# Performance work log

Measured on AMD Instinct MI355X. Metric: run time of the kernel, lower is better.

Reference implementation:

```python
import jax, jax.numpy as jnp
import numpy as np

HIDDEN = 1024
HEADS = 16
HEAD_DIM = HIDDEN // HEADS


def setup_inputs() -> dict:
    key = jax.random.key(0)
    ks = jax.random.split(key, 9)
    s = 1.0 / np.sqrt(HIDDEN)
    x = jax.random.normal(ks[0], (2, 2048, HIDDEN), dtype=jnp.float32)
    Wq = jax.random.uniform(ks[1], (HIDDEN, HIDDEN), jnp.float32, -s, s)
    bq = jax.random.uniform(ks[2], (HIDDEN,), jnp.float32, -s, s)
    Wk = jax.random.uniform(ks[3], (HIDDEN, HIDDEN), jnp.float32, -s, s)
    bk = jax.random.uniform(ks[4], (HIDDEN,), jnp.float32, -s, s)
    Wv = jax.random.uniform(ks[5], (HIDDEN, HIDDEN), jnp.float32, -s, s)
    bv = jax.random.uniform(ks[6], (HIDDEN,), jnp.float32, -s, s)
    Wo = jax.random.uniform(ks[7], (HIDDEN, HIDDEN), jnp.float32, -s, s)
    bo = jax.random.uniform(ks[8], (HIDDEN,), jnp.float32, -s, s)
    return {"x": x, "Wq": Wq, "bq": bq, "Wk": Wk, "bk": bk,
            "Wv": Wv, "bv": bv, "Wo": Wo, "bo": bo}


def reference(x, Wq, bq, Wk, bk, Wv, bv, Wo, bo):
    bs, seq_len, _ = x.shape
    # projections; weights stored as (in, out) so y = x @ W + b
    def proj(W, b):
        y = x @ W + b  # [bs, seq, hidden]
        return y.reshape(bs, seq_len, HEADS, HEAD_DIM).transpose(0, 2, 1, 3)  # [bs, h, seq, hd]
    q = proj(Wq, bq)
    k = proj(Wk, bk)
    v = proj(Wv, bv)
    scale = 1.0 / jnp.sqrt(jnp.float32(HEAD_DIM))
    scores = jnp.einsum('bhqd,bhkd->bhqk', q, k) * scale  # [bs, h, seq, seq]
    attn = jax.nn.softmax(scores, axis=-1)
    ctx = jnp.einsum('bhqk,bhkd->bhqd', attn, v)
    ctx = ctx.transpose(0, 2, 1, 3).reshape(bs, seq_len, HIDDEN)
    return ctx @ Wo + bo
```

## Files before the change

### kernel.cpp

```cpp
#include <hip/hip_runtime.h>
#include <hip/hip_bf16.h>

#define HDN 1024
#define NH  16
#define DH  64
#define NB  2
#define SQL 2048
#define MT  (NB*SQL)

using bf16 = __hip_bfloat16;
typedef __attribute__((ext_vector_type(8))) short s16x8;
typedef __attribute__((ext_vector_type(4))) float f32x4;
typedef __attribute__((ext_vector_type(16))) float f32x16;
typedef unsigned int u32;

__device__ __forceinline__ void gload_lds16(const void* g, void* l) {
  __builtin_amdgcn_global_load_lds((const __attribute__((address_space(1))) void*)g,
                                   (__attribute__((address_space(3))) void*)l, 16, 0, 0);
}

__device__ __forceinline__ unsigned short bfb(float f) {
  union { __hip_bfloat16 h; unsigned short u; } c;
  c.h = __float2bfloat16(f);
  return c.u;
}

__device__ __forceinline__ u32 cvtpk(float lo, float hi) {
  u32 r;
  asm("v_cvt_pk_bf16_f32 %0, %1, %2" : "=v"(r) : "v"(lo), "v"(hi));
  return r;
}

__global__ __launch_bounds__(256) void k_cvt_x(const float* __restrict__ x, bf16* __restrict__ xb) {
  int i = (blockIdx.x * 256 + threadIdx.x) * 8;
  float4 a = *(const float4*)(x + i);
  float4 b = *(const float4*)(x + i + 4);
  union { unsigned short u[8]; uint4 v; } o;
  o.u[0]=bfb(a.x); o.u[1]=bfb(a.y); o.u[2]=bfb(a.z); o.u[3]=bfb(a.w);
  o.u[4]=bfb(b.x); o.u[5]=bfb(b.y); o.u[6]=bfb(b.z); o.u[7]=bfb(b.w);
  *(uint4*)((unsigned short*)xb + i) = o.v;
}

__global__ __launch_bounds__(256) void k_trw(const float* __restrict__ Wq, const float* __restrict__ Wk,
                                             const float* __restrict__ Wv, const float* __restrict__ Wo,
                                             bf16* __restrict__ WqkvT, bf16* __restrict__ WoT) {
  __shared__ float tile[64][65];
  int z = blockIdx.z;
  const float* W = (z==0)?Wq:(z==1)?Wk:(z==2)?Wv:Wo;
  bf16* Wt = (z<3) ? (WqkvT + (size_t)z*HDN*HDN) : WoT;
  int r0 = blockIdx.y*64, c0 = blockIdx.x*64;
  int t = threadIdx.x, tr = t>>4, tc = (t&15)*4;
  #pragma unroll
  for (int p=0;p<4;p++){
    int r = p*16+tr;
    float4 v = *(const float4*)(W + (size_t)(r0+r)*HDN + c0 + tc);
    tile[r][tc]=v.x; tile[r][tc+1]=v.y; tile[r][tc+2]=v.z; tile[r][tc+3]=v.w;
  }
  __syncthreads();
  #pragma unroll
  for (int p=0;p<4;p++){
    int o = p*16+tr;
    union { unsigned short u[4]; ushort4 v; } pk;
    #pragma unroll
    for (int j=0;j<4;j++) pk.u[j] = bfb(tile[tc+j][o]);
    *(ushort4*)((unsigned short*)Wt + (size_t)(c0+o)*HDN + r0 + tc) = pk.v;
  }
}

template<int MODE>
__global__ __launch_bounds__(256,2) void k_gemm(
    const bf16* __restrict__ A, const bf16* __restrict__ B,
    const float* __restrict__ b0, const float* __restrict__ b1, const float* __restrict__ b2,
    bf16* __restrict__ oq, bf16* __restrict__ ok, bf16* __restrict__ ovt, float* __restrict__ oo) {
  constexpr int KD = 1024;
  __shared__ __align__(16) bf16 As[128*64];
  __shared__ __align__(16) bf16 Bs[128*64];
  int tid = threadIdx.x, lane = tid&63, wave = tid>>6;
  int g = lane>>4, lr = lane&15;
  int m0 = blockIdx.y*128, n0 = blockIdx.x*128;
  int wm = (wave>>1)*64, wn = (wave&1)*64;
  f32x4 acc[4][4] = {};
  for (int k0=0; k0<KD; k0+=64) {
    #pragma unroll
    for (int i=0;i<4;i++){
      int seg = wave*4+i;
      int flat = seg*64 + lane;
      int row = flat>>3, ch = flat&7;
      gload_lds16(A + (size_t)(m0+row)*KD + k0 + ch*8, (char*)As + seg*1024);
      gload_lds16(B + (size_t)(n0+row)*KD + k0 + ch*8, (char*)Bs + seg*1024);
    }
    __syncthreads();
    #pragma unroll
    for (int kk=0;kk<2;kk++){
      s16x8 af[4], bfg[4];
      #pragma unroll
      for (int mi=0;mi<4;mi++)
        af[mi] = *(const s16x8*)((const char*)As + (wm+mi*16+lr)*128 + kk*64 + g*16);
      #pragma unroll
      for (int ni=0;ni<4;ni++)
        bfg[ni] = *(const s16x8*)((const char*)Bs + (wn+ni*16+lr)*128 + kk*64 + g*16);
      #pragma unroll
      for (int mi=0;mi<4;mi++)
        #pragma unroll
        for (int ni=0;ni<4;ni++)
          acc[mi][ni] = __builtin_amdgcn_mfma_f32_16x16x32_bf16(af[mi], bfg[ni], acc[mi][ni], 0,0,0);
    }
    __syncthreads();
  }
  if (MODE == 0) {
    int proj = n0 >> 10;
    const float* bias = (proj==0)?b0:(proj==1)?b1:b2;
    bf16* oqk = (proj==0)?oq:ok;
    float qscale = (proj==0) ? 0.125f : 1.0f;
    #pragma unroll
    for (int ni=0;ni<4;ni++){
      int n = n0 + wn + ni*16 + lr;
      int wi = n & 1023;
      int h = wi>>6, d = wi&63;
      float bv = bias[wi];
      #pragma unroll
      for (int mi=0;mi<4;mi++){
        #pragma unroll
        for (int r=0;r<4;r++){
          int m = m0 + wm + mi*16 + g*4 + r;
          int b = m>>11, s = m&2047;
          float v = (acc[mi][ni][r] + bv) * qscale;
          if (proj<2) oqk[((size_t)((b*NH+h)*SQL + s))*DH + d] = __float2bfloat16(v);
          else        ovt[((size_t)((b*NH+h)*DH  + d))*SQL + s] = __float2bfloat16(v);
        }
      }
    }
  } else {
    #pragma unroll
    for (int ni=0;ni<4;ni++){
      int n = n0 + wn + ni*16 + lr;
      float bv = b0[n];
      #pragma unroll
      for (int mi=0;mi<4;mi++)
        #pragma unroll
        for (int r=0;r<4;r++){
          int m = m0 + wm + mi*16 + g*4 + r;
          oo[(size_t)m*HDN + n] = acc[mi][ni][r] + bv;
        }
    }
  }
}

__global__ __launch_bounds__(256,2) void k_attn(
    const bf16* __restrict__ Q, const bf16* __restrict__ K, const bf16* __restrict__ Vt,
    bf16* __restrict__ ctx) {
  __shared__ __align__(16) char sm[2][16384];
  int bh = blockIdx.x & 31, qt = blockIdx.x >> 5;
  int b = bh >> 4, h = bh & 15;
  int tid = threadIdx.x, lane = tid & 63, wv = tid >> 6;
  int cl = lane & 31, hi = lane >> 5;
  const char* Kc = (const char*)(K  + (size_t)bh*SQL*DH);
  const char* Vc = (const char*)(Vt + (size_t)bh*DH*SQL);
  const bf16* Qb = Q + (size_t)bh*SQL*DH;

  int L0 = tid*16, L1 = 4096 + tid*16;
  int r0 = L0>>7, c0 = (L0&127) ^ ((r0&7)<<4);
  int r1 = L1>>7, c1 = (L1&127) ^ ((r1&7)<<4);
  size_t kOff0 = (size_t)r0*128  + c0, kOff1 = (size_t)r1*128  + c1;
  size_t vOff0 = (size_t)r0*4096 + c0, vOff1 = (size_t)r1*4096 + c1;

  int swz = (cl&7)<<4;
  int cswz0 = (0*32 + hi*16) ^ swz;
  int cswz1 = (1*32 + hi*16) ^ swz;
  int cswz2 = (2*32 + hi*16) ^ swz;
  int cswz3 = (3*32 + hi*16) ^ swz;
  int rbase0 = cl*128;
  int rbase1 = (32+cl)*128;

  int q0 = qt*128 + wv*32;
  s16x8 qf[4];
  #pragma unroll
  for (int ds=0; ds<4; ++ds)
    qf[ds] = *(const s16x8*)((const char*)Qb + (size_t)(q0+cl)*128 + ds*32 + hi*16);

  f32x16 ca0 = {}, ca1 = {};
  float mrow = -3.0e38f, lrow = 0.f;

  auto STAGE = [&](int bb, int k0){
    char* bK = sm[bb]; char* bV = sm[bb] + 8192;
    gload_lds16(Kc + (size_t)k0*128 + kOff0, bK + wv*1024);
    gload_lds16(Kc + (size_t)k0*128 + kOff1, bK + 4096 + wv*1024);
    gload_lds16(Vc + (size_t)k0*2   + vOff0, bV + wv*1024);
    gload_lds16(Vc + (size_t)k0*2   + vOff1, bV + 4096 + wv*1024);
  };

  STAGE(0, 0);
  __syncthreads();

  for (int t=0; t<SQL/64; ++t){
    int cur = t & 1;
    if (t < SQL/64 - 1) STAGE(cur^1, (t+1)*64);
    const char* bK = sm[cur];
    const char* bV = sm[cur] + 8192;

    f32x16 s0 = {}, s1 = {};
    {
      s16x8 k00 = *(const s16x8*)(bK + rbase0 + cswz0);
      s16x8 k10 = *(const s16x8*)(bK + rbase1 + cswz0);
      s0 = __builtin_amdgcn_mfma_f32_32x32x16_bf16(k00, qf[0], s0, 0,0,0);
      s1 = __builtin_amdgcn_mfma_f32_32x32x16_bf16(k10, qf[0], s1, 0,0,0);
      s16x8 k01 = *(const s16x8*)(bK + rbase0 + cswz1);
      s16x8 k11 = *(const s16x8*)(bK + rbase1 + cswz1);
      s0 = __builtin_amdgcn_mfma_f32_32x32x16_bf16(k01, qf[1], s0, 0,0,0);
      s1 = __builtin_amdgcn_mfma_f32_32x32x16_bf16(k11, qf[1], s1, 0,0,0);
      s16x8 k02 = *(const s16x8*)(bK + rbase0 + cswz2);
      s16x8 k12 = *(const s16x8*)(bK + rbase1 + cswz2);
      s0 = __builtin_amdgcn_mfma_f32_32x32x16_bf16(k02, qf[2], s0, 0,0,0);
      s1 = __builtin_amdgcn_mfma_f32_32x32x16_bf16(k12, qf[2], s1, 0,0,0);
      s16x8 k03 = *(const s16x8*)(bK + rbase0 + cswz3);
      s16x8 k13 = *(const s16x8*)(bK + rbase1 + cswz3);
      s0 = __builtin_amdgcn_mfma_f32_32x32x16_bf16(k03, qf[3], s0, 0,0,0);
      s1 = __builtin_amdgcn_mfma_f32_32x32x16_bf16(k13, qf[3], s1, 0,0,0);
    }

    float mx = s0[0];
    #pragma unroll
    for (int i=1;i<16;i++) mx = fmaxf(mx, s0[i]);
    #pragma unroll
    for (int i=0;i<16;i++) mx = fmaxf(mx, s1[i]);
    mx = fmaxf(mx, __shfl_xor(mx, 32, 64));
    float mn = fmaxf(mrow, mx);
    float al = __expf(mrow - mn);
    mrow = mn;
    float e0[16], e1[16];
    float ls = 0.f;
    #pragma unroll
    for (int i=0;i<16;i++){ e0[i] = __expf(s0[i]-mn); ls += e0[i]; }
    #pragma unroll
    for (int i=0;i<16;i++){ e1[i] = __expf(s1[i]-mn); ls += e1[i]; }
    ls += __shfl_xor(ls, 32, 64);
    lrow = lrow*al + ls;
    #pragma unroll
    for (int i=0;i<16;i++){ ca0[i]*=al; ca1[i]*=al; }

    s16x8 pf[4];
    #pragma unroll
    for (int kb=0; kb<2; ++kb){
      const float* e = kb ? e1 : e0;
      u32 w00=cvtpk(e[0],e[1]),   w01=cvtpk(e[2],e[3]);
      u32 w10=cvtpk(e[4],e[5]),   w11=cvtpk(e[6],e[7]);
      u32 w20=cvtpk(e[8],e[9]),   w21=cvtpk(e[10],e[11]);
      u32 w30=cvtpk(e[12],e[13]), w31=cvtpk(e[14],e[15]);
      u32 sA0 = hi ? w00 : w10, sA1 = hi ? w01 : w11;
      u32 rA0 = (u32)__shfl_xor((int)sA0, 32, 64);
      u32 rA1 = (u32)__shfl_xor((int)sA1, 32, 64);
      u32 sB0 = hi ? w20 : w30, sB1 = hi ? w21 : w31;
      u32 rB0 = (u32)__shfl_xor((int)sB0, 32, 64);
      u32 rB1 = (u32)__shfl_xor((int)sB1, 32, 64);
      union { u32 u[4]; s16x8 v; } A, B;
      A.u[0] = hi?rA0:w00; A.u[1] = hi?rA1:w01; A.u[2] = hi?w10:rA0; A.u[3] = hi?w11:rA1;
      B.u[0] = hi?rB0:w20; B.u[1] = hi?rB1:w21; B.u[2] = hi?w30:rB0; B.u[3] = hi?w31:rB1;
      pf[kb*2]   = A.v;
      pf[kb*2+1] = B.v;
    }

    {
      s16x8 v00 = *(const s16x8*)(bV + rbase0 + cswz0);
      s16x8 v10 = *(const s16x8*)(bV + rbase1 + cswz0);
      ca0 = __builtin_amdgcn_mfma_f32_32x32x16_bf16(v00, pf[0], ca0, 0,0,0);
      ca1 = __builtin_amdgcn_mfma_f32_32x32x16_bf16(v10, pf[0], ca1, 0,0,0);
      s16x8 v01 = *(const s16x8*)(bV + rbase0 + cswz1);
      s16x8 v11 = *(const s16x8*)(bV + rbase1 + cswz1);
      ca0 = __builtin_amdgcn_mfma_f32_32x32x16_bf16(v01, pf[1], ca0, 0,0,0);
      ca1 = __builtin_amdgcn_mfma_f32_32x32x16_bf16(v11, pf[1], ca1, 0,0,0);
      s16x8 v02 = *(const s16x8*)(bV + rbase0 + cswz2);
      s16x8 v12 = *(const s16x8*)(bV + rbase1 + cswz2);
      ca0 = __builtin_amdgcn_mfma_f32_32x32x16_bf16(v02, pf[2], ca0, 0,0,0);
      ca1 = __builtin_amdgcn_mfma_f32_32x32x16_bf16(v12, pf[2], ca1, 0,0,0);
      s16x8 v03 = *(const s16x8*)(bV + rbase0 + cswz3);
      s16x8 v13 = *(const s16x8*)(bV + rbase1 + cswz3);
      ca0 = __builtin_amdgcn_mfma_f32_32x32x16_bf16(v03, pf[3], ca0, 0,0,0);
      ca1 = __builtin_amdgcn_mfma_f32_32x32x16_bf16(v13, pf[3], ca1, 0,0,0);
    }
    __syncthreads();
  }

  float inv = 1.f / lrow;
  char* bo = sm[0];
  int row = wv*32 + cl;
  int rswz = (row&7)<<4;
  #pragma unroll
  for (int db=0; db<2; ++db){
    #pragma unroll
    for (int r=0; r<16; r+=2){
      float va = (db ? ca1[r]   : ca0[r])   * inv;
      float vb = (db ? ca1[r+1] : ca0[r+1]) * inv;
      int d = db*32 + (r&3) + 8*(r>>2) + 4*hi;
      *(u32*)(bo + row*128 + ((d*2) ^ rswz)) = cvtpk(va, vb);
    }
  }
  __syncthreads();
  #pragma unroll
  for (int i=0;i<4;i++){
    int flat = i*256 + tid, orow = flat>>3, ch = flat&7;
    s16x8 cv = *(const s16x8*)(bo + orow*128 + ((ch*16) ^ ((orow&7)<<4)));
    *(s16x8*)(ctx + (size_t)(b*SQL + qt*128 + orow)*HDN + h*DH + ch*8) = cv;
  }
}

extern "C" void kernel_launch(void* const* d_in, const int* in_sizes, int n_in,
                              void* d_out, int out_size, void* d_ws, size_t ws_size,
                              hipStream_t stream) {
  const float* x  = (const float*)d_in[0];
  const float* Wq = (const float*)d_in[1];
  const float* bq = (const float*)d_in[2];
  const float* Wk = (const float*)d_in[3];
  const float* bk = (const float*)d_in[4];
  const float* Wv = (const float*)d_in[5];
  const float* bv = (const float*)d_in[6];
  const float* Wo = (const float*)d_in[7];
  const float* bo = (const float*)d_in[8];
  char* ws = (char*)d_ws;
  bf16* xb    = (bf16*)(ws);
  bf16* WqkvT = (bf16*)(ws + ((size_t)8<<20));
  bf16* WoT   = (bf16*)(ws + ((size_t)14<<20));
  bf16* Qg    = (bf16*)(ws + ((size_t)16<<20));
  bf16* Kg    = (bf16*)(ws + ((size_t)24<<20));
  bf16* Vtg   = (bf16*)(ws + ((size_t)32<<20));
  bf16* Ctx   = (bf16*)(ws + ((size_t)40<<20));
  float* out  = (float*)d_out;

  k_cvt_x<<<2048, 256, 0, stream>>>(x, xb);
  k_trw<<<dim3(16,16,4), 256, 0, stream>>>(Wq, Wk, Wv, Wo, WqkvT, WoT);
  k_gemm<0><<<dim3(24,32), 256, 0, stream>>>(xb, WqkvT, bq, bk, bv, Qg, Kg, Vtg, nullptr);
  k_attn<<<512, 256, 0, stream>>>(Qg, Kg, Vtg, Ctx);
  k_gemm<1><<<dim3(8,32), 256, 0, stream>>>(Ctx, WoT, bo, nullptr, nullptr,
                                            nullptr, nullptr, nullptr, out);
}
```

Measured before the change: 216.1 us.

## Split attention KV range across two warp groups and merge, with lazy rescale and exp2

The attention kernel now runs 512 threads per block. Two 256-thread groups each process half of the key/value sequence and merge their partial softmax states through LDS at the end, which doubles the waves per query tile. The softmax scale is folded into Q with a log2(e) factor so exp2f can replace __expf. Rescaling is skipped unless the running max grows by more than 8, and the cross-half shuffles become v_permlane32_swap. The cost is a larger LDS footprint, an extra merge step with more syncs, and possible occupancy limits from the doubled block size.

Result: faster. 211.9 us (-2.0%).

```diff
diff --git a/kernel.cpp b/kernel.cpp
--- a/kernel.cpp
+++ b/kernel.cpp
@@ -14,6 +14,8 @@
 typedef __attribute__((ext_vector_type(16))) float f32x16;
 typedef unsigned int u32;
 
+#define QSC 0.18033688011112042f
+
 __device__ __forceinline__ void gload_lds16(const void* g, void* l) {
   __builtin_amdgcn_global_load_lds((const __attribute__((address_space(1))) void*)g,
                                    (__attribute__((address_space(3))) void*)l, 16, 0, 0);
@@ -29,6 +31,10 @@
   u32 r;
   asm("v_cvt_pk_bf16_f32 %0, %1, %2" : "=v"(r) : "v"(lo), "v"(hi));
   return r;
+}
+
+__device__ __forceinline__ void pl32swap(u32& a, u32& b) {
+  asm("v_permlane32_swap_b32 %0, %1" : "+v"(a), "+v"(b));
 }
 
 __global__ __launch_bounds__(256) void k_cvt_x(const float* __restrict__ x, bf16* __restrict__ xb) {
@@ -111,7 +117,7 @@
     int proj = n0 >> 10;
     const float* bias = (proj==0)?b0:(proj==1)?b1:b2;
     bf16* oqk = (proj==0)?oq:ok;
-    float qscale = (proj==0) ? 0.125f : 1.0f;
+    float qscale = (proj==0) ? QSC : 1.0f;
     #pragma unroll
     for (int ni=0;ni<4;ni++){
       int n = n0 + wn + ni*16 + lr;
@@ -146,19 +152,22 @@
   }
 }
 
-__global__ __launch_bounds__(256,2) void k_attn(
+__global__ __launch_bounds__(512,4) void k_attn(
     const bf16* __restrict__ Q, const bf16* __restrict__ K, const bf16* __restrict__ Vt,
     bf16* __restrict__ ctx) {
-  __shared__ __align__(16) char sm[2][16384];
+  __shared__ __align__(16) char sm[2][2][16384];
   int bh = blockIdx.x & 31, qt = blockIdx.x >> 5;
   int b = bh >> 4, h = bh & 15;
-  int tid = threadIdx.x, lane = tid & 63, wv = tid >> 6;
+  int tid = threadIdx.x;
+  int kc = tid >> 8, tl = tid & 255;
+  int w4 = tl >> 6;
+  int lane = tid & 63;
   int cl = lane & 31, hi = lane >> 5;
   const char* Kc = (const char*)(K  + (size_t)bh*SQL*DH);
   const char* Vc = (const char*)(Vt + (size_t)bh*DH*SQL);
   const bf16* Qb = Q + (size_t)bh*SQL*DH;
 
-  int L0 = tid*16, L1 = 4096 + tid*16;
+  int L0 = tl*16, L1 = 4096 + tl*16;
   int r0 = L0>>7, c0 = (L0&127) ^ ((r0&7)<<4);
   int r1 = L1>>7, c1 = (L1&127) ^ ((r1&7)<<4);
   size_t kOff0 = (size_t)r0*128  + c0, kOff1 = (size_t)r1*128  + c1;
@@ -172,7 +181,7 @@
   int rbase0 = cl*128;
   int rbase1 = (32+cl)*128;
 
-  int q0 = qt*128 + wv*32;
+  int q0 = qt*128 + w4*32;
   s16x8 qf[4];
   #pragma unroll
   for (int ds=0; ds<4; ++ds)
@@ -181,22 +190,23 @@
   f32x16 ca0 = {}, ca1 = {};
   float mrow = -3.0e38f, lrow = 0.f;
 
-  auto STAGE = [&](int bb, int k0){
-    char* bK = sm[bb]; char* bV = sm[bb] + 8192;
-    gload_lds16(Kc + (size_t)k0*128 + kOff0, bK + wv*1024);
-    gload_lds16(Kc + (size_t)k0*128 + kOff1, bK + 4096 + wv*1024);
-    gload_lds16(Vc + (size_t)k0*2   + vOff0, bV + wv*1024);
-    gload_lds16(Vc + (size_t)k0*2   + vOff1, bV + 4096 + wv*1024);
+  auto STAGE = [&](int bb, int t){
+    int k0 = kc*1024 + t*64;
+    char* bK = &sm[kc][bb][0]; char* bV = bK + 8192;
+    gload_lds16(Kc + (size_t)k0*128 + kOff0, bK + w4*1024);
+    gload_lds16(Kc + (size_t)k0*128 + kOff1, bK + 4096 + w4*1024);
+    gload_lds16(Vc + (size_t)k0*2   + vOff0, bV + w4*1024);
+    gload_lds16(Vc + (size_t)k0*2   + vOff1, bV + 4096 + w4*1024);
   };
 
   STAGE(0, 0);
   __syncthreads();
 
-  for (int t=0; t<SQL/64; ++t){
+  for (int t=0; t<16; ++t){
     int cur = t & 1;
-    if (t < SQL/64 - 1) STAGE(cur^1, (t+1)*64);
-    const char* bK = sm[cur];
-    const char* bV = sm[cur] + 8192;
+    if (t < 15) STAGE(cur^1, t+1);
+    const char* bK = &sm[kc][cur][0];
+    const char* bV = bK + 8192;
 
     f32x16 s0 = {}, s1 = {};
     {
@@ -218,25 +228,27 @@
       s1 = __builtin_amdgcn_mfma_f32_32x32x16_bf16(k13, qf[3], s1, 0,0,0);
     }
 
-    float mx = s0[0];
-    #pragma unroll
-    for (int i=1;i<16;i++) mx = fmaxf(mx, s0[i]);
-    #pragma unroll
-    for (int i=0;i<16;i++) mx = fmaxf(mx, s1[i]);
-    mx = fmaxf(mx, __shfl_xor(mx, 32, 64));
-    float mn = fmaxf(mrow, mx);
-    float al = __expf(mrow - mn);
-    mrow = mn;
+    float pm = s0[0];
+    #pragma unroll
+    for (int i=1;i<16;i++) pm = fmaxf(pm, s0[i]);
+    #pragma unroll
+    for (int i=0;i<16;i++) pm = fmaxf(pm, s1[i]);
+    pm = fmaxf(pm, __shfl_xor(pm, 32, 64));
+    if (!__all(pm <= mrow + 8.f)) {
+      float mn = fmaxf(mrow, pm);
+      float al = exp2f(mrow - mn);
+      mrow = mn;
+      lrow *= al;
+      #pragma unroll
+      for (int i=0;i<16;i++){ ca0[i]*=al; ca1[i]*=al; }
+    }
     float e0[16], e1[16];
     float ls = 0.f;
     #pragma unroll
-    for (int i=0;i<16;i++){ e0[i] = __expf(s0[i]-mn); ls += e0[i]; }
-    #pragma unroll
-    for (int i=0;i<16;i++){ e1[i] = __expf(s1[i]-mn); ls += e1[i]; }
-    ls += __shfl_xor(ls, 32, 64);
-    lrow = lrow*al + ls;
-    #pragma unroll
-    for (int i=0;i<16;i++){ ca0[i]*=al; ca1[i]*=al; }
+    for (int i=0;i<16;i++){ e0[i] = exp2f(s0[i]-mrow); ls += e0[i]; }
+    #pragma unroll
+    for (int i=0;i<16;i++){ e1[i] = exp2f(s1[i]-mrow); ls += e1[i]; }
+    lrow += ls;
 
     s16x8 pf[4];
     #pragma unroll
@@ -246,15 +258,13 @@
       u32 w10=cvtpk(e[4],e[5]),   w11=cvtpk(e[6],e[7]);
       u32 w20=cvtpk(e[8],e[9]),   w21=cvtpk(e[10],e[11]);
       u32 w30=cvtpk(e[12],e[13]), w31=cvtpk(e[14],e[15]);
-      u32 sA0 = hi ? w00 : w10, sA1 = hi ? w01 : w11;
-      u32 rA0 = (u32)__shfl_xor((int)sA0, 32, 64);
-      u32 rA1 = (u32)__shfl_xor((int)sA1, 32, 64);
-      u32 sB0 = hi ? w20 : w30, sB1 = hi ? w21 : w31;
-      u32 rB0 = (u32)__shfl_xor((int)sB0, 32, 64);
-      u32 rB1 = (u32)__shfl_xor((int)sB1, 32, 64);
+      pl32swap(w00, w10);
+      pl32swap(w01, w11);
+      pl32swap(w20, w30);
+      pl32swap(w21, w31);
       union { u32 u[4]; s16x8 v; } A, B;
-      A.u[0] = hi?rA0:w00; A.u[1] = hi?rA1:w01; A.u[2] = hi?w10:rA0; A.u[3] = hi?w11:rA1;
-      B.u[0] = hi?rB0:w20; B.u[1] = hi?rB1:w21; B.u[2] = hi?w30:rB0; B.u[3] = hi?w31:rB1;
+      A.u[0]=w00; A.u[1]=w01; A.u[2]=w10; A.u[3]=w11;
+      B.u[0]=w20; B.u[1]=w21; B.u[2]=w30; B.u[3]=w31;
       pf[kb*2]   = A.v;
       pf[kb*2+1] = B.v;
     }
@@ -280,26 +290,51 @@
     __syncthreads();
   }
 
-  float inv = 1.f / lrow;
-  char* bo = sm[0];
-  int row = wv*32 + cl;
-  int rswz = (row&7)<<4;
-  #pragma unroll
-  for (int db=0; db<2; ++db){
-    #pragma unroll
-    for (int r=0; r<16; r+=2){
-      float va = (db ? ca1[r]   : ca0[r])   * inv;
-      float vb = (db ? ca1[r+1] : ca0[r+1]) * inv;
-      int d = db*32 + (r&3) + 8*(r>>2) + 4*hi;
-      *(u32*)(bo + row*128 + ((d*2) ^ rswz)) = cvtpk(va, vb);
-    }
-  }
-  __syncthreads();
-  #pragma unroll
-  for (int i=0;i<4;i++){
-    int flat = i*256 + tid, orow = flat>>3, ch = flat&7;
-    s16x8 cv = *(const s16x8*)(bo + orow*128 + ((ch*16) ^ ((orow&7)<<4)));
-    *(s16x8*)(ctx + (size_t)(b*SQL + qt*128 + orow)*HDN + h*DH + ch*8) = cv;
+  lrow += __shfl_xor(lrow, 32, 64);
+
+  char*  base = &sm[0][0][0];
+  float* mlb  = (float*)(base + 16384);
+  float* o2b  = (float*)(base + 32768);
+  char*  cb   = base;
+
+  __syncthreads();
+  if (kc == 1) {
+    if (!hi) { mlb[(w4*32+cl)*2] = mrow; mlb[(w4*32+cl)*2+1] = lrow; }
+    #pragma unroll
+    for (int db=0; db<2; ++db)
+      #pragma unroll
+      for (int r=0; r<16; ++r){
+        int d = db*32 + (r&3) + 8*(r>>2) + 4*hi;
+        o2b[w4*2048 + d*32 + cl] = db ? ca1[r] : ca0[r];
+      }
+  }
+  __syncthreads();
+  if (kc == 0) {
+    float m2 = mlb[(w4*32+cl)*2], l2 = mlb[(w4*32+cl)*2+1];
+    float M  = fmaxf(mrow, m2);
+    float a1 = exp2f(mrow - M), a2 = exp2f(m2 - M);
+    float inv = 1.f / (lrow*a1 + l2*a2);
+    int row = w4*32 + cl;
+    int rswz = (row&7)<<4;
+    #pragma unroll
+    for (int db=0; db<2; ++db){
+      #pragma unroll
+      for (int r=0; r<16; r+=2){
+        int d = db*32 + (r&3) + 8*(r>>2) + 4*hi;
+        float va = ((db?ca1[r]:ca0[r])  *a1 + o2b[w4*2048 + d*32     + cl]*a2) * inv;
+        float vb = ((db?ca1[r+1]:ca0[r+1])*a1 + o2b[w4*2048 + (d+1)*32 + cl]*a2) * inv;
+        *(u32*)(cb + row*128 + ((d*2) ^ rswz)) = cvtpk(va, vb);
+      }
+    }
+  }
+  __syncthreads();
+  if (kc == 0) {
+    #pragma unroll
+    for (int i=0;i<4;i++){
+      int flat = i*256 + tl, orow = flat>>3, ch = flat&7;
+      s16x8 cv = *(const s16x8*)(cb + orow*128 + ((ch*16) ^ ((orow&7)<<4)));
+      *(s16x8*)(ctx + (size_t)(b*SQL + qt*128 + orow)*HDN + h*DH + ch*8) = cv;
+    }
   }
 }
 
@@ -328,7 +363,7 @@
   k_cvt_x<<<2048, 256, 0, stream>>>(x, xb);
   k_trw<<<dim3(16,16,4), 256, 0, stream>>>(Wq, Wk, Wv, Wo, WqkvT, WoT);
   k_gemm<0><<<dim3(24,32), 256, 0, stream>>>(xb, WqkvT, bq, bk, bv, Qg, Kg, Vtg, nullptr);
-  k_attn<<<512, 256, 0, stream>>>(Qg, Kg, Vtg, Ctx);
+  k_attn<<<512, 512, 0, stream>>>(Qg, Kg, Vtg, Ctx);
   k_gemm<1><<<dim3(8,32), 256, 0, stream>>>(Ctx, WoT, bo, nullptr, nullptr,
                                             nullptr, nullptr, nullptr, out);
 }
```
